# Kernel tuning notes

Measured on AMD Instinct MI355X. Metric: run time of the kernel, lower is better.

The kernel has to match this reference:

```python
import jax, jax.numpy as jnp
import numpy as np

N, NFEAT, NHID, NCLASS, NLAYERS = 10000, 512, 256, 40, 8
LAMDA, ALPHA = 0.5, 0.1
EDGE_P = 0.003  # avg degree ~30


def setup_inputs() -> dict:
    key = jax.random.key(0)
    ks = jax.random.split(key, 8)
    x = jax.random.normal(ks[0], (N, NFEAT), dtype=jnp.float32)
    # binary adjacency with zero diagonal (normalize_adj asserts diag==0)
    adj = (jax.random.uniform(ks[1], (N, N)) < EDGE_P).astype(jnp.float32)
    adj = adj * (1.0 - jnp.eye(N, dtype=jnp.float32))
    # GraphConvolution.reset_parameters: uniform(-1/sqrt(out), 1/sqrt(out))
    s = 1.0 / np.sqrt(NHID)
    conv_w = jax.random.uniform(ks[2], (NLAYERS, NHID, NHID), jnp.float32, -s, s)
    s0 = 1.0 / np.sqrt(NFEAT)
    w0 = jax.random.uniform(ks[3], (NFEAT, NHID), jnp.float32, -s0, s0)
    b0 = jax.random.uniform(ks[4], (NHID,), jnp.float32, -s0, s0)
    s1 = 1.0 / np.sqrt(NHID)
    w1 = jax.random.uniform(ks[5], (NHID, NCLASS), jnp.float32, -s1, s1)
    b1 = jax.random.uniform(ks[6], (NCLASS,), jnp.float32, -s1, s1)
    return {"x": x, "adj": adj, "w0": w0, "b0": b0, "conv_w": conv_w, "w1": w1, "b1": b1}


def reference(x, adj, w0, b0, conv_w, w1, b1):
    n = adj.shape[0]
    # normalize_adj: A_hat = A + I; D^{-1/2} A_hat D^{-1/2}
    a_hat = adj + jnp.eye(n, dtype=adj.dtype)
    d_inv_sqrt = jax.lax.rsqrt(jnp.sum(a_hat, axis=1))
    a_norm = a_hat * d_inv_sqrt[:, None] * d_inv_sqrt[None, :]

    # dropout is a no-op in eval mode
    h0 = jax.nn.relu(x @ w0 + b0)  # [N, NHID]
    thetas = jnp.log(LAMDA / jnp.arange(1, NLAYERS + 1, dtype=jnp.float32) + 1.0)

    def step(h, wt):
        w, theta = wt
        hi = a_norm @ h                              # aggregation
        support = (1.0 - ALPHA) * hi + ALPHA * h0    # initial-residual mix (variant=False: r = support)
        out = theta * (support @ w) + (1.0 - theta) * support
        return jax.nn.relu(out), None

    h, _ = jax.lax.scan(step, h0, (conv_w, thetas))
    logits = h @ w1 + b1  # [N, NCLASS]
    return jax.nn.log_softmax(logits, axis=1)
```

## Files before the change

kernel.cpp:

```cpp
#include <hip/hip_runtime.h>
#include <math.h>

#define NN 10000
#define NFEAT 512
#define NHID 256
#define NCLASS 40
#define NLAYERS 8
#define MAXDEG 96

typedef __attribute__((ext_vector_type(8))) short bf16x8;
typedef __attribute__((ext_vector_type(4))) float floatx4;
typedef __attribute__((ext_vector_type(2))) float floatx2;
typedef __attribute__((ext_vector_type(4))) unsigned short ushort4v;

__device__ __forceinline__ unsigned short f2bf(float f) {
    union { float f; unsigned int u; } v; v.f = f;
    unsigned int r = v.u + 0x7fffu + ((v.u >> 16) & 1u);
    return (unsigned short)(r >> 16);
}
__device__ __forceinline__ float bf2f(unsigned short h) {
    union { unsigned int u; float f; } v; v.u = ((unsigned int)h) << 16;
    return v.f;
}
__device__ __forceinline__ unsigned char f2fp8(float f) {
    return (unsigned char)(__builtin_amdgcn_cvt_pk_fp8_f32(f, f, 0, false) & 0xFF);
}

__global__ __launch_bounds__(256) void build_graph(const float* __restrict__ adj,
                                                   int* __restrict__ cnt,
                                                   int* __restrict__ ell,
                                                   float* __restrict__ dinv) {
    int i = blockIdx.x;
    __shared__ int scnt;
    if (threadIdx.x == 0) scnt = 0;
    __syncthreads();
    const float4* row = (const float4*)(adj + (size_t)i * NN);
    const int nv = NN / 4;
    int* erow = ell + (size_t)i * MAXDEG;
    for (int f = threadIdx.x; f < nv; f += 256) {
        float4 v = row[f];
        if (v.x != 0.0f) { int s = atomicAdd(&scnt, 1); if (s < MAXDEG) erow[s] = 4*f + 0; }
        if (v.y != 0.0f) { int s = atomicAdd(&scnt, 1); if (s < MAXDEG) erow[s] = 4*f + 1; }
        if (v.z != 0.0f) { int s = atomicAdd(&scnt, 1); if (s < MAXDEG) erow[s] = 4*f + 2; }
        if (v.w != 0.0f) { int s = atomicAdd(&scnt, 1); if (s < MAXDEG) erow[s] = 4*f + 3; }
    }
    __syncthreads();
    if (threadIdx.x == 0) {
        int c = scnt;
        cnt[i] = (c < MAXDEG) ? c : MAXDEG;
        dinv[i] = rsqrtf(1.0f + (float)c);
    }
}

__global__ __launch_bounds__(256) void prep_ell(int* __restrict__ ell,
                                                const int* __restrict__ cnt,
                                                const float* __restrict__ dinv,
                                                float* __restrict__ scl_g) {
    int idx = blockIdx.x * 256 + threadIdx.x;
    if (idx >= NN * MAXDEG) return;
    int i = idx / MAXDEG, e = idx % MAXDEG;
    if (e < cnt[i]) {
        scl_g[idx] = dinv[ell[idx]];
    } else {
        scl_g[idx] = 0.0f;
        ell[idx] = 0;
    }
}

__global__ __launch_bounds__(256) void convert_x(const float* __restrict__ x,
                                                 unsigned short* __restrict__ xb) {
    int idx = blockIdx.x * 256 + threadIdx.x;
    float4 v = ((const float4*)x)[idx];
    ushort4v o;
    o.x = f2bf(v.x); o.y = f2bf(v.y); o.z = f2bf(v.z); o.w = f2bf(v.w);
    ((ushort4v*)xb)[idx] = o;
}

__global__ __launch_bounds__(256) void convert_h8(const unsigned short* __restrict__ hb,
                                                  unsigned int* __restrict__ h8) {
    int idx = blockIdx.x * 256 + threadIdx.x;
    ushort4v v = ((const ushort4v*)hb)[idx];
    unsigned int p = __builtin_amdgcn_cvt_pk_fp8_f32(bf2f(v.x), bf2f(v.y), 0, false);
    p = __builtin_amdgcn_cvt_pk_fp8_f32(bf2f(v.z), bf2f(v.w), p, true);
    h8[idx] = p;
}

__global__ __launch_bounds__(256) void prep_weights(const float* __restrict__ w0,
                                                    const float* __restrict__ cw,
                                                    unsigned short* __restrict__ w0t,
                                                    unsigned short* __restrict__ Mt) {
    int idx = blockIdx.x * 256 + threadIdx.x;
    if (idx < 131072) {
        int n = idx >> 9, k = idx & 511;
        w0t[idx] = f2bf(w0[(size_t)k * 256 + n]);
    } else {
        int j = idx - 131072;
        int l = j >> 16;
        int r = j & 65535;
        int n = r >> 8, k = r & 255;
        float theta = logf(0.5f / (float)(l + 1) + 1.0f);
        float v = theta * cw[(size_t)l * 65536 + (size_t)k * 256 + n];
        if (k == n) v += 1.0f - theta;
        Mt[j] = f2bf(v);
    }
}

__global__ __launch_bounds__(512, 4) void gemm0_mfma(const unsigned short* __restrict__ xb,
                                                     const unsigned short* __restrict__ w0t,
                                                     const float* __restrict__ b0,
                                                     unsigned short* __restrict__ h0b) {
    int t = threadIdx.x, wv = t >> 6, lane = t & 63;
    int lrow = lane & 15, quad = lane >> 4;
    int r0 = blockIdx.x * 16;

    bf16x8 a[16];
    const unsigned short* arow = xb + (size_t)(r0 + lrow) * NFEAT + quad * 8;
    #pragma unroll
    for (int f = 0; f < 16; ++f)
        a[f] = *(const bf16x8*)(arow + f * 32);

    #pragma unroll 1
    for (int n = 0; n < 2; ++n) {
        int nt = wv * 2 + n;
        floatx4 acc = {0.f, 0.f, 0.f, 0.f};
        const unsigned short* wrow = w0t + (size_t)(nt * 16 + lrow) * NFEAT + quad * 8;
        #pragma unroll
        for (int f = 0; f < 16; ++f) {
            bf16x8 b = *(const bf16x8*)(wrow + f * 32);
            acc = __builtin_amdgcn_mfma_f32_16x16x32_bf16(a[f], b, acc, 0, 0, 0);
        }
        int col = nt * 16 + lrow;
        float bias = b0[col];
        #pragma unroll
        for (int r = 0; r < 4; ++r) {
            int row = r0 + quad * 4 + r;
            h0b[(size_t)row * NHID + col] = f2bf(fmaxf(acc[r] + bias, 0.f));
        }
    }
}

template<bool LAST>
__global__ __launch_bounds__(512, 6) void layer_fused(const unsigned int* __restrict__ h8,
                                                      const unsigned short* __restrict__ h0b,
                                                      const float* __restrict__ dinv,
                                                      const int* __restrict__ cnt,
                                                      const int* __restrict__ ell,
                                                      const float* __restrict__ scl_g,
                                                      const unsigned short* __restrict__ Mt,
                                                      const float* __restrict__ w1,
                                                      const float* __restrict__ b1,
                                                      unsigned char* __restrict__ h8_out,
                                                      float* __restrict__ out) {
    __shared__ unsigned short supb[16][264];
    __shared__ float hs[LAST ? 16 * 264 : 4];

    int t = threadIdx.x;
    int wv = __builtin_amdgcn_readfirstlane(t >> 6);
    int lane = t & 63;
    int r0 = blockIdx.x * 16;

    #pragma unroll 1
    for (int rr = 0; rr < 2; ++rr) {
        int lr = wv * 2 + rr;
        int i  = r0 + lr;
        int deg8 = (cnt[i] + 7) & ~7;
        float di = dinv[i];
        const int*   ellrow = ell   + (size_t)i * MAXDEG;
        const float* sclrow = scl_g + (size_t)i * MAXDEG;
        unsigned int su = h8[(size_t)i * 64 + lane];
        floatx2 slo = __builtin_amdgcn_cvt_pk_f32_fp8(su, false);
        floatx2 shi = __builtin_amdgcn_cvt_pk_f32_fp8(su, true);
        float4 acc;
        acc.x = di * slo.x;
        acc.y = di * slo.y;
        acc.z = di * shi.x;
        acc.w = di * shi.y;
        #pragma unroll 1
        for (int e0 = 0; e0 < deg8; e0 += 8) {
            #pragma unroll
            for (int u = 0; u < 8; ++u) {
                int   j = ellrow[e0 + u];
                float s = sclrow[e0 + u];
                unsigned int xu = h8[(size_t)j * 64 + lane];
                floatx2 lo = __builtin_amdgcn_cvt_pk_f32_fp8(xu, false);
                floatx2 hi = __builtin_amdgcn_cvt_pk_f32_fp8(xu, true);
                acc.x = fmaf(s, lo.x, acc.x);
                acc.y = fmaf(s, lo.y, acc.y);
                acc.z = fmaf(s, hi.x, acc.z);
                acc.w = fmaf(s, hi.y, acc.w);
            }
        }
        ushort4v h0v = ((const ushort4v*)h0b)[(size_t)i * 64 + lane];
        ushort4v ob;
        ob.x = f2bf(0.9f * (di * acc.x) + 0.1f * bf2f(h0v.x));
        ob.y = f2bf(0.9f * (di * acc.y) + 0.1f * bf2f(h0v.y));
        ob.z = f2bf(0.9f * (di * acc.z) + 0.1f * bf2f(h0v.z));
        ob.w = f2bf(0.9f * (di * acc.w) + 0.1f * bf2f(h0v.w));
        *(ushort4v*)&supb[lr][4 * lane] = ob;
    }
    __syncthreads();

    int lrow = lane & 15, quad = lane >> 4;
    bf16x8 a[8];
    #pragma unroll
    for (int f = 0; f < 8; ++f)
        a[f] = *(const bf16x8*)&supb[lrow][quad * 8 + f * 32];

    #pragma unroll 1
    for (int n = 0; n < 2; ++n) {
        int nt = wv * 2 + n;
        floatx4 acc = {0.f, 0.f, 0.f, 0.f};
        const unsigned short* wrow = Mt + (size_t)(nt * 16 + lrow) * NHID + quad * 8;
        #pragma unroll
        for (int f = 0; f < 8; ++f) {
            bf16x8 b = *(const bf16x8*)(wrow + f * 32);
            acc = __builtin_amdgcn_mfma_f32_16x16x32_bf16(a[f], b, acc, 0, 0, 0);
        }
        int col = nt * 16 + lrow;
        #pragma unroll
        for (int r = 0; r < 4; ++r) {
            int lr2 = quad * 4 + r;
            float o = fmaxf(acc[r], 0.f);
            if (LAST) {
                hs[lr2 * 264 + col] = o;
            } else {
                h8_out[(size_t)(r0 + lr2) * NHID + col] = f2fp8(o);
            }
        }
    }

    if (LAST) {
        __syncthreads();
        #pragma unroll 1
        for (int rr = 0; rr < 2; ++rr) {
            int lr = wv * 2 + rr;
            const float* hr = hs + lr * 264;
            float logit = -1e30f;
            if (lane < NCLASS) {
                float acc = b1[lane];
                #pragma unroll 8
                for (int k = 0; k < NHID; ++k)
                    acc = fmaf(hr[k], w1[k * NCLASS + lane], acc);
                logit = acc;
            }
            float m = logit;
            #pragma unroll
            for (int off = 32; off > 0; off >>= 1)
                m = fmaxf(m, __shfl_xor(m, off, 64));
            float e = (lane < NCLASS) ? expf(logit - m) : 0.0f;
            float ssum = e;
            #pragma unroll
            for (int off = 32; off > 0; off >>= 1)
                ssum += __shfl_xor(ssum, off, 64);
            float lse = m + logf(ssum);
            if (lane < NCLASS)
                out[(size_t)(r0 + lr) * NCLASS + lane] = logit - lse;
        }
    }
}

extern "C" void kernel_launch(void* const* d_in, const int* in_sizes, int n_in,
                              void* d_out, int out_size, void* d_ws, size_t ws_size,
                              hipStream_t stream) {
    const float* x      = (const float*)d_in[0];
    const float* adj    = (const float*)d_in[1];
    const float* w0     = (const float*)d_in[2];
    const float* b0     = (const float*)d_in[3];
    const float* conv_w = (const float*)d_in[4];
    const float* w1     = (const float*)d_in[5];
    const float* b1     = (const float*)d_in[6];
    float* out = (float*)d_out;

    char* ws = (char*)d_ws;
    size_t off = 0;
    auto alloc = [&](size_t bytes) -> void* {
        void* p = ws + off;
        off = (off + bytes + 255) & ~(size_t)255;
        return p;
    };
    float*          dinv  = (float*)alloc((size_t)NN * 4);
    int*            cnt   = (int*)  alloc((size_t)NN * 4);
    int*            ell   = (int*)  alloc((size_t)NN * MAXDEG * 4);
    float*          scl_g = (float*)alloc((size_t)NN * MAXDEG * 4);
    unsigned short* xb    = (unsigned short*)alloc((size_t)NN * NFEAT * 2);
    unsigned short* w0t   = (unsigned short*)alloc((size_t)NFEAT * NHID * 2);
    unsigned short* Mt    = (unsigned short*)alloc((size_t)NLAYERS * NHID * NHID * 2);
    unsigned short* h0b   = (unsigned short*)alloc((size_t)NN * NHID * 2);
    unsigned int*   h08   = (unsigned int*)alloc((size_t)NN * NHID);
    unsigned int*   hP8   = (unsigned int*)alloc((size_t)NN * NHID);
    unsigned int*   hQ8   = (unsigned int*)alloc((size_t)NN * NHID);

    build_graph<<<NN, 256, 0, stream>>>(adj, cnt, ell, dinv);
    convert_x<<<(NN * NFEAT / 4) / 256, 256, 0, stream>>>(x, xb);
    prep_weights<<<(131072 + NLAYERS * NHID * NHID) / 256, 256, 0, stream>>>(w0, conv_w, w0t, Mt);
    prep_ell<<<(NN * MAXDEG + 255) / 256, 256, 0, stream>>>(ell, cnt, dinv, scl_g);

    gemm0_mfma<<<NN / 16, 512, 0, stream>>>(xb, w0t, b0, h0b);
    convert_h8<<<(NN * NHID / 4) / 256, 256, 0, stream>>>(h0b, h08);

    const unsigned int* hc8 = h08;
    for (int l = 0; l < NLAYERS; ++l) {
        unsigned int* nxt = (l & 1) ? hQ8 : hP8;
        const unsigned short* wt = Mt + (size_t)l * NHID * NHID;
        if (l == NLAYERS - 1)
            layer_fused<true><<<NN / 16, 512, 0, stream>>>(hc8, h0b, dinv, cnt, ell, scl_g, wt, w1, b1, nullptr, out);
        else
            layer_fused<false><<<NN / 16, 512, 0, stream>>>(hc8, h0b, dinv, cnt, ell, scl_g, wt, nullptr, nullptr, (unsigned char*)nxt, nullptr);
        hc8 = nxt;
    }
}
```

Measured before the change: 780.8 us.

## Software-pipeline two-row ELL gather and fuse fp8 conversion into gemm0

The aggregation loop now processes both rows of each wave together and double-buffers groups of eight neighbor loads, so gathers for the next group are in flight while the current group is accumulated. Neighbor indices and scales are packed into one int2 array, so each edge needs one load instead of two. The separate fp8 conversion kernel is removed by writing the fp8 copy directly in the gemm0 epilogue. In exchange, register pressure rises from the four staging buffers, and both rows iterate to the larger of the two degrees, relying on zero-padded entries.

```diff
diff --git a/kernel.cpp b/kernel.cpp
--- a/kernel.cpp
+++ b/kernel.cpp
@@ -52,19 +52,19 @@
     }
 }
 
-__global__ __launch_bounds__(256) void prep_ell(int* __restrict__ ell,
+__global__ __launch_bounds__(256) void prep_ell(const int* __restrict__ ell,
                                                 const int* __restrict__ cnt,
                                                 const float* __restrict__ dinv,
-                                                float* __restrict__ scl_g) {
+                                                int2* __restrict__ es) {
     int idx = blockIdx.x * 256 + threadIdx.x;
     if (idx >= NN * MAXDEG) return;
     int i = idx / MAXDEG, e = idx % MAXDEG;
+    int2 v; v.x = 0; v.y = 0;
     if (e < cnt[i]) {
-        scl_g[idx] = dinv[ell[idx]];
-    } else {
-        scl_g[idx] = 0.0f;
-        ell[idx] = 0;
-    }
+        int j = ell[idx];
+        v.x = j; v.y = __float_as_int(dinv[j]);
+    }
+    es[idx] = v;
 }
 
 __global__ __launch_bounds__(256) void convert_x(const float* __restrict__ x,
@@ -74,15 +74,6 @@
     ushort4v o;
     o.x = f2bf(v.x); o.y = f2bf(v.y); o.z = f2bf(v.z); o.w = f2bf(v.w);
     ((ushort4v*)xb)[idx] = o;
-}
-
-__global__ __launch_bounds__(256) void convert_h8(const unsigned short* __restrict__ hb,
-                                                  unsigned int* __restrict__ h8) {
-    int idx = blockIdx.x * 256 + threadIdx.x;
-    ushort4v v = ((const ushort4v*)hb)[idx];
-    unsigned int p = __builtin_amdgcn_cvt_pk_fp8_f32(bf2f(v.x), bf2f(v.y), 0, false);
-    p = __builtin_amdgcn_cvt_pk_fp8_f32(bf2f(v.z), bf2f(v.w), p, true);
-    h8[idx] = p;
 }
 
 __global__ __launch_bounds__(256) void prep_weights(const float* __restrict__ w0,
@@ -108,7 +99,8 @@
 __global__ __launch_bounds__(512, 4) void gemm0_mfma(const unsigned short* __restrict__ xb,
                                                      const unsigned short* __restrict__ w0t,
                                                      const float* __restrict__ b0,
-                                                     unsigned short* __restrict__ h0b) {
+                                                     unsigned short* __restrict__ h0b,
+                                                     unsigned char* __restrict__ h8o) {
     int t = threadIdx.x, wv = t >> 6, lane = t & 63;
     int lrow = lane & 15, quad = lane >> 4;
     int r0 = blockIdx.x * 16;
@@ -134,8 +126,48 @@
         #pragma unroll
         for (int r = 0; r < 4; ++r) {
             int row = r0 + quad * 4 + r;
-            h0b[(size_t)row * NHID + col] = f2bf(fmaxf(acc[r] + bias, 0.f));
-        }
+            unsigned short bv = f2bf(fmaxf(acc[r] + bias, 0.f));
+            h0b[(size_t)row * NHID + col] = bv;
+            h8o[(size_t)row * NHID + col] = f2fp8(bf2f(bv));
+        }
+    }
+}
+
+__device__ __forceinline__ void load_group(const int2* __restrict__ e0r,
+                                           const int2* __restrict__ e1r,
+                                           const unsigned int* __restrict__ h8,
+                                           int lane, int base,
+                                           unsigned int (&x0)[8], unsigned int (&x1)[8],
+                                           float (&s0)[8], float (&s1)[8]) {
+    #pragma unroll
+    for (int u = 0; u < 8; ++u) {
+        int2 p = e0r[base + u];
+        int2 q = e1r[base + u];
+        s0[u] = __int_as_float(p.y);
+        s1[u] = __int_as_float(q.y);
+        x0[u] = h8[(size_t)p.x * 64 + lane];
+        x1[u] = h8[(size_t)q.x * 64 + lane];
+    }
+}
+
+__device__ __forceinline__ void proc_group(const unsigned int (&x0)[8],
+                                           const unsigned int (&x1)[8],
+                                           const float (&s0)[8], const float (&s1)[8],
+                                           float4& a0, float4& a1) {
+    #pragma unroll
+    for (int u = 0; u < 8; ++u) {
+        floatx2 lo = __builtin_amdgcn_cvt_pk_f32_fp8(x0[u], false);
+        floatx2 hi = __builtin_amdgcn_cvt_pk_f32_fp8(x0[u], true);
+        a0.x = fmaf(s0[u], lo.x, a0.x);
+        a0.y = fmaf(s0[u], lo.y, a0.y);
+        a0.z = fmaf(s0[u], hi.x, a0.z);
+        a0.w = fmaf(s0[u], hi.y, a0.w);
+        lo = __builtin_amdgcn_cvt_pk_f32_fp8(x1[u], false);
+        hi = __builtin_amdgcn_cvt_pk_f32_fp8(x1[u], true);
+        a1.x = fmaf(s1[u], lo.x, a1.x);
+        a1.y = fmaf(s1[u], lo.y, a1.y);
+        a1.z = fmaf(s1[u], hi.x, a1.z);
+        a1.w = fmaf(s1[u], hi.y, a1.w);
     }
 }
 
@@ -144,8 +176,7 @@
                                                       const unsigned short* __restrict__ h0b,
                                                       const float* __restrict__ dinv,
                                                       const int* __restrict__ cnt,
-                                                      const int* __restrict__ ell,
-                                                      const float* __restrict__ scl_g,
+                                                      const int2* __restrict__ es,
                                                       const unsigned short* __restrict__ Mt,
                                                       const float* __restrict__ w1,
                                                       const float* __restrict__ b1,
@@ -159,45 +190,58 @@
     int lane = t & 63;
     int r0 = blockIdx.x * 16;
 
+    int lr0 = wv * 2, lr1 = lr0 + 1;
+    int i0 = r0 + lr0, i1 = r0 + lr1;
+
+    unsigned int su0 = h8[(size_t)i0 * 64 + lane];
+    unsigned int su1 = h8[(size_t)i1 * 64 + lane];
+    ushort4v h0v0 = ((const ushort4v*)h0b)[(size_t)i0 * 64 + lane];
+    ushort4v h0v1 = ((const ushort4v*)h0b)[(size_t)i1 * 64 + lane];
+
+    float di0 = dinv[i0], di1 = dinv[i1];
+    int dA = (cnt[i0] + 7) & ~7, dB = (cnt[i1] + 7) & ~7;
+    int dm = dA > dB ? dA : dB;
+    const int2* e0r = es + (size_t)i0 * MAXDEG;
+    const int2* e1r = es + (size_t)i1 * MAXDEG;
+
+    floatx2 slo = __builtin_amdgcn_cvt_pk_f32_fp8(su0, false);
+    floatx2 shi = __builtin_amdgcn_cvt_pk_f32_fp8(su0, true);
+    float4 a0, a1;
+    a0.x = di0 * slo.x; a0.y = di0 * slo.y; a0.z = di0 * shi.x; a0.w = di0 * shi.y;
+    slo = __builtin_amdgcn_cvt_pk_f32_fp8(su1, false);
+    shi = __builtin_amdgcn_cvt_pk_f32_fp8(su1, true);
+    a1.x = di1 * slo.x; a1.y = di1 * slo.y; a1.z = di1 * shi.x; a1.w = di1 * shi.y;
+
+    unsigned int xA0[8], xA1[8], xB0[8], xB1[8];
+    float sA0[8], sA1[8], sB0[8], sB1[8];
+    int ng = dm >> 3;
+    load_group(e0r, e1r, h8, lane, 0, xA0, xA1, sA0, sA1);
+    bool useA = true;
     #pragma unroll 1
-    for (int rr = 0; rr < 2; ++rr) {
-        int lr = wv * 2 + rr;
-        int i  = r0 + lr;
-        int deg8 = (cnt[i] + 7) & ~7;
-        float di = dinv[i];
-        const int*   ellrow = ell   + (size_t)i * MAXDEG;
-        const float* sclrow = scl_g + (size_t)i * MAXDEG;
-        unsigned int su = h8[(size_t)i * 64 + lane];
-        floatx2 slo = __builtin_amdgcn_cvt_pk_f32_fp8(su, false);
-        floatx2 shi = __builtin_amdgcn_cvt_pk_f32_fp8(su, true);
-        float4 acc;
-        acc.x = di * slo.x;
-        acc.y = di * slo.y;
-        acc.z = di * shi.x;
-        acc.w = di * shi.y;
-        #pragma unroll 1
-        for (int e0 = 0; e0 < deg8; e0 += 8) {
-            #pragma unroll
-            for (int u = 0; u < 8; ++u) {
-                int   j = ellrow[e0 + u];
-                float s = sclrow[e0 + u];
-                unsigned int xu = h8[(size_t)j * 64 + lane];
-                floatx2 lo = __builtin_amdgcn_cvt_pk_f32_fp8(xu, false);
-                floatx2 hi = __builtin_amdgcn_cvt_pk_f32_fp8(xu, true);
-                acc.x = fmaf(s, lo.x, acc.x);
-                acc.y = fmaf(s, lo.y, acc.y);
-                acc.z = fmaf(s, hi.x, acc.z);
-                acc.w = fmaf(s, hi.y, acc.w);
-            }
-        }
-        ushort4v h0v = ((const ushort4v*)h0b)[(size_t)i * 64 + lane];
-        ushort4v ob;
-        ob.x = f2bf(0.9f * (di * acc.x) + 0.1f * bf2f(h0v.x));
-        ob.y = f2bf(0.9f * (di * acc.y) + 0.1f * bf2f(h0v.y));
-        ob.z = f2bf(0.9f * (di * acc.z) + 0.1f * bf2f(h0v.z));
-        ob.w = f2bf(0.9f * (di * acc.w) + 0.1f * bf2f(h0v.w));
-        *(ushort4v*)&supb[lr][4 * lane] = ob;
-    }
+    for (int g = 1; g < ng; ++g) {
+        if (useA) {
+            load_group(e0r, e1r, h8, lane, g << 3, xB0, xB1, sB0, sB1);
+            proc_group(xA0, xA1, sA0, sA1, a0, a1);
+        } else {
+            load_group(e0r, e1r, h8, lane, g << 3, xA0, xA1, sA0, sA1);
+            proc_group(xB0, xB1, sB0, sB1, a0, a1);
+        }
+        useA = !useA;
+    }
+    if (useA) proc_group(xA0, xA1, sA0, sA1, a0, a1);
+    else      proc_group(xB0, xB1, sB0, sB1, a0, a1);
+
+    ushort4v ob;
+    ob.x = f2bf(0.9f * (di0 * a0.x) + 0.1f * bf2f(h0v0.x));
+    ob.y = f2bf(0.9f * (di0 * a0.y) + 0.1f * bf2f(h0v0.y));
+    ob.z = f2bf(0.9f * (di0 * a0.z) + 0.1f * bf2f(h0v0.z));
+    ob.w = f2bf(0.9f * (di0 * a0.w) + 0.1f * bf2f(h0v0.w));
+    *(ushort4v*)&supb[lr0][4 * lane] = ob;
+    ob.x = f2bf(0.9f * (di1 * a1.x) + 0.1f * bf2f(h0v1.x));
+    ob.y = f2bf(0.9f * (di1 * a1.y) + 0.1f * bf2f(h0v1.y));
+    ob.z = f2bf(0.9f * (di1 * a1.z) + 0.1f * bf2f(h0v1.z));
+    ob.w = f2bf(0.9f * (di1 * a1.w) + 0.1f * bf2f(h0v1.w));
+    *(ushort4v*)&supb[lr1][4 * lane] = ob;
     __syncthreads();
 
     int lrow = lane & 15, quad = lane >> 4;
@@ -281,7 +325,7 @@
     float*          dinv  = (float*)alloc((size_t)NN * 4);
     int*            cnt   = (int*)  alloc((size_t)NN * 4);
     int*            ell   = (int*)  alloc((size_t)NN * MAXDEG * 4);
-    float*          scl_g = (float*)alloc((size_t)NN * MAXDEG * 4);
+    int2*           es    = (int2*) alloc((size_t)NN * MAXDEG * 8);
     unsigned short* xb    = (unsigned short*)alloc((size_t)NN * NFEAT * 2);
     unsigned short* w0t   = (unsigned short*)alloc((size_t)NFEAT * NHID * 2);
     unsigned short* Mt    = (unsigned short*)alloc((size_t)NLAYERS * NHID * NHID * 2);
@@ -293,19 +337,17 @@
     build_graph<<<NN, 256, 0, stream>>>(adj, cnt, ell, dinv);
     convert_x<<<(NN * NFEAT / 4) / 256, 256, 0, stream>>>(x, xb);
     prep_weights<<<(131072 + NLAYERS * NHID * NHID) / 256, 256, 0, stream>>>(w0, conv_w, w0t, Mt);
-    prep_ell<<<(NN * MAXDEG + 255) / 256, 256, 0, stream>>>(ell, cnt, dinv, scl_g);
-
-    gemm0_mfma<<<NN / 16, 512, 0, stream>>>(xb, w0t, b0, h0b);
-    convert_h8<<<(NN * NHID / 4) / 256, 256, 0, stream>>>(h0b, h08);
+    prep_ell<<<(NN * MAXDEG + 255) / 256, 256, 0, stream>>>(ell, cnt, dinv, es);
+    gemm0_mfma<<<NN / 16, 512, 0, stream>>>(xb, w0t, b0, h0b, (unsigned char*)h08);
 
     const unsigned int* hc8 = h08;
     for (int l = 0; l < NLAYERS; ++l) {
         unsigned int* nxt = (l & 1) ? hQ8 : hP8;
         const unsigned short* wt = Mt + (size_t)l * NHID * NHID;
         if (l == NLAYERS - 1)
-            layer_fused<true><<<NN / 16, 512, 0, stream>>>(hc8, h0b, dinv, cnt, ell, scl_g, wt, w1, b1, nullptr, out);
+            layer_fused<true><<<NN / 16, 512, 0, stream>>>(hc8, h0b, dinv, cnt, es, wt, w1, b1, nullptr, out);
         else
-            layer_fused<false><<<NN / 16, 512, 0, stream>>>(hc8, h0b, dinv, cnt, ell, scl_g, wt, nullptr, nullptr, (unsigned char*)nxt, nullptr);
+            layer_fused<false><<<NN / 16, 512, 0, stream>>>(hc8, h0b, dinv, cnt, es, wt, nullptr, nullptr, (unsigned char*)nxt, nullptr);
         hc8 = nxt;
     }
 }
```

New measurement: 852.0 us. +9.1%, slower.
